# Optimization experiments

Measured on AMD Instinct MI355X. Metric: run time of the kernel, lower is better.

The kernel has to match this reference:

```python
import jax, jax.numpy as jnp
import numpy as np
import math

B, S, D, H, MLP, L = 4, 1024, 512, 8, 2048, 4
C = D // H  # head dim = 64
K_RATIO = 0.25
TOPK = max(1, min(S, int(math.ceil(K_RATIO * S))))  # 256
EPS = 1e-6


def layernorm(x, w, b):
    mu = jnp.mean(x, axis=-1, keepdims=True)
    var = jnp.mean(jnp.square(x - mu), axis=-1, keepdims=True)
    return (x - mu) * jax.lax.rsqrt(var + EPS) * w + b


def dwconv3(x, w):
    # x: (B, Ch, S), w: (Ch, 1, 3) depthwise conv, padding 1
    return jax.lax.conv_general_dilated(
        x, w, window_strides=(1,), padding=[(1, 1)],
        dimension_numbers=('NCH', 'OIH', 'NCH'),
        feature_group_count=x.shape[1])


def setup_inputs() -> dict:
    key = jax.random.key(0)
    ks = jax.random.split(key, 16)
    g = lambda k, shape, s=0.02: jax.random.normal(k, shape, jnp.float32) * s
    return {
        'x': jax.random.normal(ks[0], (B, S, D), jnp.float32),
        'pos_emb': g(ks[1], (1, S, D)),
        'ln1_w': jnp.ones((L, D), jnp.float32),
        'ln1_b': jnp.zeros((L, D), jnp.float32),
        'qkv_w': g(ks[2], (L, 3 * D, D)),
        'dw_w': g(ks[3], (L, 3 * D, 1, 3), 0.1),
        'temp': jnp.ones((L, H), jnp.float32),
        'proj_w': g(ks[4], (L, D, D)),
        'ln2_w': jnp.ones((L, D), jnp.float32),
        'ln2_b': jnp.zeros((L, D), jnp.float32),
        'mlp_w1': g(ks[5], (L, MLP, D)),
        'mlp_b1': g(ks[6], (L, MLP), 1e-6),
        'mlp_w2': g(ks[7], (L, D, MLP)),
        'mlp_b2': g(ks[8], (L, D), 1e-6),
        'lnf_w': jnp.ones((D,), jnp.float32),
        'lnf_b': jnp.zeros((D,), jnp.float32),
    }


def _block(x, ln1_w, ln1_b, qkv_w, dw_w, temp, proj_w, ln2_w, ln2_b,
           mlp_w1, mlp_b1, mlp_w2, mlp_b2):
    # x: (B, S, D)
    h = layernorm(x, ln1_w, ln1_b).swapaxes(1, 2)        # (B, D, S)
    qkv = jnp.einsum('od,bds->bos', qkv_w, h)            # (B, 3D, S) 1x1 conv
    qkv = dwconv3(qkv, dw_w)                             # depthwise k=3
    q, k, v = jnp.split(qkv, 3, axis=1)                  # each (B, D, S)
    # 'b (head c) s -> b head s c'
    to_heads = lambda t: t.reshape(B, H, C, S).transpose(0, 1, 3, 2)
    q, k, v = to_heads(q), to_heads(k), to_heads(v)      # (B, H, S, C)
    q = q / jnp.maximum(jnp.linalg.norm(q, axis=-1, keepdims=True), 1e-12)
    k = k / jnp.maximum(jnp.linalg.norm(k, axis=-1, keepdims=True), 1e-12)
    scores = jnp.einsum('bhsc,bhtc->bhst', q, k) * temp[None, :, None, None]
    # top-k per query row: keep entries >= k-th largest, mask rest to -inf
    kth = jax.lax.top_k(scores, TOPK)[0][..., -1:]       # (B, H, S, 1)
    sparse = jnp.where(scores >= kth, scores, -jnp.inf)
    sparse = jnp.clip(sparse, -10000.0, 10000.0)         # -inf -> -10000
    attn = jax.nn.softmax(sparse, axis=-1)
    out = jnp.einsum('bhst,bhtc->bhsc', attn, v)         # (B, H, S, C)
    out = out.transpose(0, 1, 3, 2).reshape(B, D, S)     # 'b head s c -> b (head c) s'
    out = jnp.einsum('od,bds->bos', proj_w, out)         # project_out 1x1 conv
    x = x + out.swapaxes(1, 2)                           # residual (dropout=0)
    y = layernorm(x, ln2_w, ln2_b)
    y = jax.nn.gelu(y @ mlp_w1.T + mlp_b1, approximate=False) @ mlp_w2.T + mlp_b2
    return x + y


def reference(x, pos_emb, ln1_w, ln1_b, qkv_w, dw_w, temp, proj_w,
              ln2_w, ln2_b, mlp_w1, mlp_b1, mlp_w2, mlp_b2, lnf_w, lnf_b):
    h = x + pos_emb
    for i in range(L):
        h = _block(h, ln1_w[i], ln1_b[i], qkv_w[i], dw_w[i], temp[i], proj_w[i],
                   ln2_w[i], ln2_b[i], mlp_w1[i], mlp_b1[i], mlp_w2[i], mlp_b2[i])
    return layernorm(h, lnf_w, lnf_b)
```

## Files before the change

### kernel.cpp

```cpp
#include <hip/hip_runtime.h>

#define NB   4
#define SEQ  1024
#define DIM  512
#define NH   8
#define HD   64
#define MLPD 2048
#define NL   4
#define TOPKK 256
#define QKVD 1536
#define QT   16

typedef short bh8 __attribute__((ext_vector_type(8)));
typedef float f32x4 __attribute__((ext_vector_type(4)));

__device__ __forceinline__ float b2f(unsigned short v) {
    return __uint_as_float(((unsigned)v) << 16);
}
__device__ __forceinline__ unsigned short f2b(float f) {
    unsigned u = __float_as_uint(f);
    u += 0x7FFFu + ((u >> 16) & 1u);
    return (unsigned short)(u >> 16);
}
__device__ __forceinline__ float ldin(const void* p, size_t i, int bf) {
    return bf ? b2f(((const unsigned short*)p)[i]) : ((const float*)p)[i];
}
__device__ __forceinline__ float wave_sum(float v) {
#pragma unroll
    for (int m = 32; m; m >>= 1) v += __shfl_xor(v, m);
    return v;
}
__device__ __forceinline__ unsigned f2key16(unsigned short u) {
    return (u & 0x8000u) ? (unsigned)((~u) & 0xFFFFu) : (unsigned)(u | 0x8000u);
}
__device__ __forceinline__ unsigned short key16b(unsigned k) {
    return (k & 0x8000u) ? (unsigned short)(k & 0x7FFFu)
                         : (unsigned short)((~k) & 0xFFFFu);
}
__device__ __forceinline__ unsigned cvtpk(float a, float b) {
    unsigned r;
    asm("v_cvt_pk_bf16_f32 %0, %1, %2" : "=v"(r) : "v"(a), "v"(b));
    return r;
}
__device__ __forceinline__ uint4 pack8(const float* __restrict__ p) {
    uint4 r;
    r.x = (unsigned)f2b(p[0]) | ((unsigned)f2b(p[1]) << 16);
    r.y = (unsigned)f2b(p[2]) | ((unsigned)f2b(p[3]) << 16);
    r.z = (unsigned)f2b(p[4]) | ((unsigned)f2b(p[5]) << 16);
    r.w = (unsigned)f2b(p[6]) | ((unsigned)f2b(p[7]) << 16);
    return r;
}
__device__ __forceinline__ void async16(unsigned short* lds, const unsigned short* g) {
    __builtin_amdgcn_global_load_lds(
        (const __attribute__((address_space(1))) unsigned int*)g,
        (__attribute__((address_space(3))) unsigned int*)lds, 16, 0, 0);
}


__global__ void detect_kernel(const unsigned short* __restrict__ ln1w,
                              int* __restrict__ flag) {
    if (threadIdx.x == 0 && blockIdx.x == 0)
        *flag = (ln1w[0] == 0x3F80u) ? 1 : 0;
}

__global__ __launch_bounds__(256) void wcvt_kernel(
    const void* __restrict__ W, unsigned short* __restrict__ out,
    int n, const int* __restrict__ dflag) {
    int bf = *dflag;
    int idx = blockIdx.x * 256 + threadIdx.x;
    if (idx < n) out[idx] = f2b(ldin(W, idx, bf));
}

__global__ __launch_bounds__(256) void addpos_kernel(
    const void* __restrict__ x, const void* __restrict__ pos,
    float* __restrict__ h, const int* __restrict__ dflag) {
    int bf = *dflag;
    int idx = blockIdx.x * 256 + threadIdx.x;
    int sd = idx & (SEQ * DIM - 1);
    h[idx] = ldin(x, idx, bf) + ldin(pos, sd, bf);
}

__global__ __launch_bounds__(256) void ln_kernel(
    const float* __restrict__ in, const void* __restrict__ w,
    const void* __restrict__ bb, size_t wo, unsigned short* __restrict__ out,
    const int* __restrict__ dflag) {
    int bf = *dflag;
    int tid = threadIdx.x;
    int lane = tid & 63, wid = tid >> 6;
    int row = blockIdx.x * 4 + wid;
    const float* p = in + (size_t)row * DIM + lane * 8;
    float4 x0 = *(const float4*)(p);
    float4 x1 = *(const float4*)(p + 4);
    float d[8] = {x0.x, x0.y, x0.z, x0.w, x1.x, x1.y, x1.z, x1.w};
    float s = (d[0] + d[1]) + (d[2] + d[3]) + (d[4] + d[5]) + (d[6] + d[7]);
    s = wave_sum(s);
    float mean = s * (1.0f / DIM);
    float q = 0.f;
#pragma unroll
    for (int j = 0; j < 8; ++j) {
        d[j] -= mean;
        q += d[j] * d[j];
    }
    q = wave_sum(q);
    float rs = rsqrtf(q * (1.0f / DIM) + 1e-6f);
    size_t eo = wo + lane * 8;
    unsigned short* o = out + (size_t)row * DIM + lane * 8;
    unsigned pw[4];
#pragma unroll
    for (int j = 0; j < 4; ++j) {
        float v0 = d[2 * j]     * rs * ldin(w, eo + 2 * j, bf)     + ldin(bb, eo + 2 * j, bf);
        float v1 = d[2 * j + 1] * rs * ldin(w, eo + 2 * j + 1, bf) + ldin(bb, eo + 2 * j + 1, bf);
        pw[j] = (unsigned)f2b(v0) | ((unsigned)f2b(v1) << 16);
    }
    *(uint4*)o = (uint4){pw[0], pw[1], pw[2], pw[3]};
}

__global__ __launch_bounds__(256) void lnf_kernel(
    const float* __restrict__ in, const void* __restrict__ w,
    const void* __restrict__ bb, void* __restrict__ out,
    const int* __restrict__ dflag) {
    int bf = *dflag;
    __shared__ float red[4];
    int row = blockIdx.x, tid = threadIdx.x;
    int lane = tid & 63, wid = tid >> 6;
    const float* p = in + (size_t)row * DIM;
    float x0 = p[tid], x1 = p[tid + 256];
    float s = wave_sum(x0 + x1);
    if (!lane) red[wid] = s;
    __syncthreads();
    float mean = (red[0] + red[1] + red[2] + red[3]) * (1.0f / DIM);
    float d0 = x0 - mean, d1 = x1 - mean;
    float q = wave_sum(d0 * d0 + d1 * d1);
    __syncthreads();
    if (!lane) red[wid] = q;
    __syncthreads();
    float var = (red[0] + red[1] + red[2] + red[3]) * (1.0f / DIM);
    float rs = rsqrtf(var + 1e-6f);
    float v0 = d0 * rs * ldin(w, tid, bf) + ldin(bb, tid, bf);
    float v1 = d1 * rs * ldin(w, tid + 256, bf) + ldin(bb, tid + 256, bf);
    size_t o = (size_t)row * DIM;
    if (bf) {
        ((unsigned short*)out)[o + tid]       = f2b(v0);
        ((unsigned short*)out)[o + tid + 256] = f2b(v1);
    } else {
        ((float*)out)[o + tid]       = v0;
        ((float*)out)[o + tid + 256] = v1;
    }
}

__global__ __launch_bounds__(256) void gemm_mfma_kernel(
    const unsigned short* __restrict__ A, const void* __restrict__ W, size_t wo,
    const void* __restrict__ bias, size_t bo, void* __restrict__ C,
    int M, int N, int K, int flags, const int* __restrict__ dflag) {
    int bf = *dflag;
    __shared__ unsigned short As[128 * 32];
    __shared__ unsigned short Bs[128 * 32];
    int tid = threadIdx.x;
    int w = tid >> 6, l = tid & 63;
    int n0 = blockIdx.x * 128, m0 = blockIdx.y * 128;
    int wm = (w >> 1) * 64, wn = (w & 1) * 64;
    int lq = l & 15, lk = l >> 4;

    int srow = w * 32 + (l >> 2);
    int cb = (l & 3) * 8;
    const unsigned short* aG = A + (size_t)(m0 + srow) * K + cb;
    size_t wb = wo + (size_t)(n0 + srow) * K + cb;
    unsigned short* sA0 = &As[w * 1024 + l * 8];
    unsigned short* sA1 = &As[w * 1024 + 512 + l * 8];
    unsigned short* sB0 = &Bs[w * 1024 + l * 8];
    unsigned short* sB1 = &Bs[w * 1024 + 512 + l * 8];

    f32x4 acc[4][4];
#pragma unroll
    for (int i = 0; i < 4; ++i)
#pragma unroll
        for (int j = 0; j < 4; ++j)
            acc[i][j] = (f32x4){0.f, 0.f, 0.f, 0.f};

    for (int k0 = 0; k0 < K; k0 += 32) {
        uint4 a0 = *(const uint4*)(aG + k0);
        uint4 a1 = *(const uint4*)(aG + 16 * K + k0);
        uint4 b0, b1;
        if (bf) {
            b0 = *(const uint4*)((const unsigned short*)W + wb + k0);
            b1 = *(const uint4*)((const unsigned short*)W + wb + 16 * K + k0);
        } else {
            b0 = pack8((const float*)W + wb + k0);
            b1 = pack8((const float*)W + wb + 16 * K + k0);
        }
        __syncthreads();
        *(uint4*)sA0 = a0;
        *(uint4*)sA1 = a1;
        *(uint4*)sB0 = b0;
        *(uint4*)sB1 = b1;
        __syncthreads();
        bh8 af[4], bw[4];
#pragma unroll
        for (int i = 0; i < 4; ++i) {
            af[i] = *(const bh8*)&As[(wm + i * 16 + lq) * 32 + lk * 8];
            bw[i] = *(const bh8*)&Bs[(wn + i * 16 + lq) * 32 + lk * 8];
        }
#pragma unroll
        for (int i = 0; i < 4; ++i)
#pragma unroll
            for (int j = 0; j < 4; ++j)
                acc[i][j] = __builtin_amdgcn_mfma_f32_16x16x32_bf16(
                    af[i], bw[j], acc[i][j], 0, 0, 0);
    }

    int lr4 = lk * 4;
#pragma unroll
    for (int i = 0; i < 4; ++i) {
#pragma unroll
        for (int j = 0; j < 4; ++j) {
            int n = n0 + wn + j * 16 + lq;
            float bv = (flags & 4) ? ldin(bias, bo + n, bf) : 0.0f;
#pragma unroll
            for (int r = 0; r < 4; ++r) {
                int m = m0 + wm + i * 16 + lr4 + r;
                float v = acc[i][j][r] + bv;
                if (flags & 2) v = 0.5f * v * (1.0f + erff(v * 0.70710678118654752f));
                size_t o = (size_t)m * N + n;
                if (flags & 1) ((float*)C)[o] += v;
                else           ((unsigned short*)C)[o] = f2b(v);
            }
        }
    }
}

__global__ __launch_bounds__(256) void gemm_mfma_n64_kernel(
    const unsigned short* __restrict__ A, const void* __restrict__ W, size_t wo,
    const void* __restrict__ bias, size_t bo, void* __restrict__ C,
    int M, int N, int K, int flags, const int* __restrict__ dflag) {
    int bf = *dflag;
    __shared__ unsigned short As[128 * 32];
    __shared__ unsigned short Bs[64 * 32];
    int tid = threadIdx.x;
    int w = tid >> 6, l = tid & 63;
    int n0 = blockIdx.x * 64, m0 = blockIdx.y * 128;
    int wm = (w >> 1) * 64, wn = (w & 1) * 32;
    int lq = l & 15, lk = l >> 4;

    int srowA = w * 32 + (l >> 2);
    int cb = (l & 3) * 8;
    const unsigned short* aG = A + (size_t)(m0 + srowA) * K + cb;
    int srowB = w * 16 + (l >> 2);
    size_t wb = wo + (size_t)(n0 + srowB) * K + cb;
    unsigned short* sA0 = &As[w * 1024 + l * 8];
    unsigned short* sA1 = &As[w * 1024 + 512 + l * 8];
    unsigned short* sB0 = &Bs[w * 512 + l * 8];

    f32x4 acc[4][2];
#pragma unroll
    for (int i = 0; i < 4; ++i) {
        acc[i][0] = (f32x4){0.f, 0.f, 0.f, 0.f};
        acc[i][1] = (f32x4){0.f, 0.f, 0.f, 0.f};
    }

    for (int k0 = 0; k0 < K; k0 += 32) {
        uint4 a0 = *(const uint4*)(aG + k0);
        uint4 a1 = *(const uint4*)(aG + 16 * K + k0);
        uint4 b0;
        if (bf) b0 = *(const uint4*)((const unsigned short*)W + wb + k0);
        else    b0 = pack8((const float*)W + wb + k0);
        __syncthreads();
        *(uint4*)sA0 = a0;
        *(uint4*)sA1 = a1;
        *(uint4*)sB0 = b0;
        __syncthreads();
        bh8 af[4], bw[2];
#pragma unroll
        for (int i = 0; i < 4; ++i)
            af[i] = *(const bh8*)&As[(wm + i * 16 + lq) * 32 + lk * 8];
        bw[0] = *(const bh8*)&Bs[(wn + lq) * 32 + lk * 8];
        bw[1] = *(const bh8*)&Bs[(wn + 16 + lq) * 32 + lk * 8];
#pragma unroll
        for (int i = 0; i < 4; ++i) {
            acc[i][0] = __builtin_amdgcn_mfma_f32_16x16x32_bf16(af[i], bw[0], acc[i][0], 0, 0, 0);
            acc[i][1] = __builtin_amdgcn_mfma_f32_16x16x32_bf16(af[i], bw[1], acc[i][1], 0, 0, 0);
        }
    }

    int lr4 = lk * 4;
#pragma unroll
    for (int i = 0; i < 4; ++i) {
#pragma unroll
        for (int j = 0; j < 2; ++j) {
            int n = n0 + wn + j * 16 + lq;
            float bv = (flags & 4) ? ldin(bias, bo + n, bf) : 0.0f;
#pragma unroll
            for (int r = 0; r < 4; ++r) {
                int m = m0 + wm + i * 16 + lr4 + r;
                float v = acc[i][j][r] + bv;
                if (flags & 2) v = 0.5f * v * (1.0f + erff(v * 0.70710678118654752f));
                size_t o = (size_t)m * N + n;
                if (flags & 1) ((float*)C)[o] += v;
                else           ((unsigned short*)C)[o] = f2b(v);
            }
        }
    }
}

__global__ __launch_bounds__(256) void gemm_n64_dlds_kernel(
    const unsigned short* __restrict__ A, const unsigned short* __restrict__ W, size_t wo,
    const void* __restrict__ bias, size_t bo, void* __restrict__ C,
    int M, int N, int K, int flags, const int* __restrict__ dflag) {
    __shared__ unsigned short As[128 * 32];
    __shared__ unsigned short Bs[64 * 32];
    int tid = threadIdx.x;
    int w = tid >> 6, l = tid & 63;
    int n0 = blockIdx.x * 64, m0 = blockIdx.y * 128;
    int kz = blockIdx.z;
    int Ks = K / (int)gridDim.z;
    int kbeg = kz * Ks, kend = kbeg + Ks;
    int wm = (w >> 1) * 64, wn = (w & 1) * 32;
    int lq = l & 15, lk = l >> 4;

    int srowA = w * 32 + (l >> 2);
    int srowB = w * 16 + (l >> 2);
    int cb = (l & 3) * 8;
    const unsigned short* aG = A + (size_t)(m0 + srowA) * K + cb;
    const unsigned short* wG = W + wo + (size_t)(n0 + srowB) * K + cb;
    unsigned short* lA0 = As + w * 1024;
    unsigned short* lA1 = As + w * 1024 + 512;
    unsigned short* lB0 = Bs + w * 512;

    f32x4 acc[4][2];
#pragma unroll
    for (int i = 0; i < 4; ++i) {
        acc[i][0] = (f32x4){0.f, 0.f, 0.f, 0.f};
        acc[i][1] = (f32x4){0.f, 0.f, 0.f, 0.f};
    }

    for (int k0 = kbeg; k0 < kend; k0 += 32) {
        __syncthreads();
        async16(lA0, aG + k0);
        async16(lA1, aG + 16 * K + k0);
        async16(lB0, wG + k0);
        __syncthreads();
        bh8 af[4], bw[2];
#pragma unroll
        for (int i = 0; i < 4; ++i)
            af[i] = *(const bh8*)&As[(wm + i * 16 + lq) * 32 + lk * 8];
        bw[0] = *(const bh8*)&Bs[(wn + lq) * 32 + lk * 8];
        bw[1] = *(const bh8*)&Bs[(wn + 16 + lq) * 32 + lk * 8];
#pragma unroll
        for (int i = 0; i < 4; ++i) {
            acc[i][0] = __builtin_amdgcn_mfma_f32_16x16x32_bf16(af[i], bw[0], acc[i][0], 0, 0, 0);
            acc[i][1] = __builtin_amdgcn_mfma_f32_16x16x32_bf16(af[i], bw[1], acc[i][1], 0, 0, 0);
        }
    }

    int bf = (flags & 4) ? *dflag : 0;
    int lr4 = lk * 4;
#pragma unroll
    for (int i = 0; i < 4; ++i) {
#pragma unroll
        for (int j = 0; j < 2; ++j) {
            int n = n0 + wn + j * 16 + lq;
            float bv = ((flags & 4) && kz == 0) ? ldin(bias, bo + n, bf) : 0.0f;
#pragma unroll
            for (int r = 0; r < 4; ++r) {
                int m = m0 + wm + i * 16 + lr4 + r;
                float v = acc[i][j][r] + bv;
                if (flags & 2) v = 0.5f * v * (1.0f + erff(v * 0.70710678118654752f));
                size_t o = (size_t)m * N + n;
                if (flags & 8)      atomicAdd(&((float*)C)[o], v);
                else if (flags & 1) ((float*)C)[o] += v;
                else                ((unsigned short*)C)[o] = f2b(v);
            }
        }
    }
}

__global__ __launch_bounds__(256) void dwqkv_kernel(
    const unsigned short* __restrict__ in, const void* __restrict__ w, size_t wo,
    const void* __restrict__ temp, size_t to,
    unsigned short* __restrict__ qn, unsigned short* __restrict__ Kc,
    unsigned short* __restrict__ Vt, const int* __restrict__ dflag) {
    int bf = *dflag;
    int tid = threadIdx.x;
    int g = tid >> 6, c = tid & 63;
    int gid = blockIdx.x * 4 + g;
    int h = gid & 7;
    int bs = gid >> 3;
    int s = bs & (SEQ - 1), b = bs >> 10;
    int bh = b * NH + h;
    const unsigned short* row = in + (size_t)bs * QKVD;
    float vals[3];
#pragma unroll
    for (int t = 0; t < 3; ++t) {
        int o = t * 512 + h * HD + c;
        float w0 = ldin(w, wo + o * 3 + 0, bf);
        float w1 = ldin(w, wo + o * 3 + 1, bf);
        float w2 = ldin(w, wo + o * 3 + 2, bf);
        float a = w1 * b2f(row[o]);
        if (s > 0)       a += w0 * b2f(row[o - QKVD]);
        if (s < SEQ - 1) a += w2 * b2f(row[o + QKVD]);
        vals[t] = a;
    }
    float qs = wave_sum(vals[0] * vals[0]);
    float ks = wave_sum(vals[1] * vals[1]);
    float t_ = ldin(temp, to + h, bf);
    qn[(size_t)bs * DIM + h * HD + c] = f2b(vals[0] / fmaxf(sqrtf(qs), 1e-12f) * t_);
    Kc[((size_t)bh * SEQ + s) * HD + c] = f2b(vals[1] / fmaxf(sqrtf(ks), 1e-12f));
    Vt[(((size_t)bh * 32 + (s >> 5)) * HD + c) * 32 + (s & 31)] = f2b(vals[2]);
}

__global__ __launch_bounds__(256) void attn_kernel(
    const unsigned short* __restrict__ q, const unsigned short* __restrict__ Kc,
    const unsigned short* __restrict__ Vt, unsigned short* __restrict__ outp) {
    __shared__ __align__(16) unsigned short sc16[QT * 1024];

    int tid = threadIdx.x;
    int w = tid >> 6, l = tid & 63;
    int lq = l & 15, lk = l >> 4;
    int bid = blockIdx.x;
    int qt = (bid >> 3) & 63;
    int bh = ((bid >> 9) << 3) | (bid & 7);
    int h = bh & 7;
    int b = bh >> 3;

    const unsigned short* qp = q + (size_t)(b * SEQ + qt * QT + lq) * DIM + h * HD + lk * 8;
    bh8 aq0 = *(const bh8*)(qp);
    bh8 aq1 = *(const bh8*)(qp + 32);

    int swz = ((lq ^ (lq >> 2)) & 7) << 1;

    const unsigned short* Kbh = Kc + (size_t)bh * SEQ * HD;
    unsigned short* srowq = sc16 + lq * 1024;
    for (int kb = 0; kb < 16; kb += 2) {
        int key0 = (w * 16 + kb) * 16;
        const unsigned short* kp0 = Kbh + (size_t)(key0 + lq) * HD + lk * 8;
        const unsigned short* kp1 = kp0 + 16 * HD;
        bh8 b0 = *(const bh8*)(kp0);
        bh8 b1 = *(const bh8*)(kp0 + 32);
        bh8 b2 = *(const bh8*)(kp1);
        bh8 b3 = *(const bh8*)(kp1 + 32);
        f32x4 a0 = {0.f, 0.f, 0.f, 0.f};
        f32x4 a1 = {0.f, 0.f, 0.f, 0.f};
        a0 = __builtin_amdgcn_mfma_f32_16x16x32_bf16(b0, aq0, a0, 0, 0, 0);
        a0 = __builtin_amdgcn_mfma_f32_16x16x32_bf16(b1, aq1, a0, 0, 0, 0);
        a1 = __builtin_amdgcn_mfma_f32_16x16x32_bf16(b2, aq0, a1, 0, 0, 0);
        a1 = __builtin_amdgcn_mfma_f32_16x16x32_bf16(b3, aq1, a1, 0, 0, 0);
        int c0 = (key0 >> 2) + lk;
        uint2 w0 = {cvtpk(a0[0], a0[1]), cvtpk(a0[2], a0[3])};
        uint2 w1 = {cvtpk(a1[0], a1[1]), cvtpk(a1[2], a1[3])};
        *(uint2*)&srowq[(c0 ^ swz) << 2]       = w0;
        *(uint2*)&srowq[((c0 + 4) ^ swz) << 2] = w1;
    }
    __syncthreads();

    for (int rr = 0; rr < 4; rr += 2) {
        int rowA = w * 4 + rr;
        unsigned short* sAr = sc16 + rowA * 1024;
        unsigned short* sBr = sc16 + (rowA + 1) * 1024;
        uint4 ra0 = *(const uint4*)&sAr[l * 8];
        uint4 ra1 = *(const uint4*)&sAr[512 + l * 8];
        uint4 rb0 = *(const uint4*)&sBr[l * 8];
        uint4 rb1 = *(const uint4*)&sBr[512 + l * 8];
        unsigned wa[8] = {ra0.x, ra0.y, ra0.z, ra0.w, ra1.x, ra1.y, ra1.z, ra1.w};
        unsigned wb[8] = {rb0.x, rb0.y, rb0.z, rb0.w, rb1.x, rb1.y, rb1.z, rb1.w};
        float va[16], vb[16];
#pragma unroll
        for (int j = 0; j < 8; ++j) {
            va[2 * j]     = __uint_as_float(wa[j] << 16);
            va[2 * j + 1] = __uint_as_float(wa[j] & 0xFFFF0000u);
            vb[2 * j]     = __uint_as_float(wb[j] << 16);
            vb[2 * j + 1] = __uint_as_float(wb[j] & 0xFFFF0000u);
        }
        float ma = va[0], mb = vb[0];
#pragma unroll
        for (int j = 1; j < 16; ++j) {
            ma = fmaxf(ma, va[j]);
            mb = fmaxf(mb, vb[j]);
        }
#pragma unroll
        for (int off = 1; off < 64; off <<= 1) {
            ma = fmaxf(ma, __shfl_xor(ma, off));
            mb = fmaxf(mb, __shfl_xor(mb, off));
        }
        ma = fminf(fmaxf(ma, -10000.f), 10000.f);
        mb = fminf(fmaxf(mb, -10000.f), 10000.f);
        unsigned Ta = 0, Tb = 0;
        for (int bit = 15; bit >= 0; --bit) {
            unsigned ca = Ta | (1u << bit), cb = Tb | (1u << bit);
            float tfa = b2f(key16b(ca)), tfb = b2f(key16b(cb));
            unsigned cna = 0, cnb = 0;
#pragma unroll
            for (int j = 0; j < 16; ++j) {
                cna += (unsigned)__popcll(__ballot(va[j] >= tfa));
                cnb += (unsigned)__popcll(__ballot(vb[j] >= tfb));
            }
            if (cna >= TOPKK) Ta = ca;
            if (cnb >= TOPKK) Tb = cb;
        }
        float ka = b2f(key16b(Ta)), kb = b2f(key16b(Tb));
        float sa = 0.f, sb = 0.f;
#pragma unroll
        for (int j = 0; j < 16; ++j) {
            float aa = fminf(fmaxf(va[j], -10000.f), 10000.f);
            float ab = fminf(fmaxf(vb[j], -10000.f), 10000.f);
            float ea = (va[j] >= ka) ? __expf(aa - ma) : 0.0f;
            float eb = (vb[j] >= kb) ? __expf(ab - mb) : 0.0f;
            sa += ea; sb += eb;
            va[j] = ea; vb[j] = eb;
        }
#pragma unroll
        for (int off = 1; off < 64; off <<= 1) {
            sa += __shfl_xor(sa, off);
            sb += __shfl_xor(sb, off);
        }
        float ia = 1.0f / sa, ib = 1.0f / sb;
        unsigned pa[8], pb[8];
#pragma unroll
        for (int j = 0; j < 8; ++j) {
            pa[j] = cvtpk(va[2 * j] * ia, va[2 * j + 1] * ia);
            pb[j] = cvtpk(vb[2 * j] * ib, vb[2 * j + 1] * ib);
        }
        *(uint4*)&sAr[l * 8]       = (uint4){pa[0], pa[1], pa[2], pa[3]};
        *(uint4*)&sAr[512 + l * 8] = (uint4){pa[4], pa[5], pa[6], pa[7]};
        *(uint4*)&sBr[l * 8]       = (uint4){pb[0], pb[1], pb[2], pb[3]};
        *(uint4*)&sBr[512 + l * 8] = (uint4){pb[4], pb[5], pb[6], pb[7]};
    }
    __syncthreads();

    {
        const unsigned short* Vbh = Vt + (size_t)bh * SEQ * HD;
        const unsigned short* prow = sc16 + lq * 1024;
        f32x4 oacc = {0.f, 0.f, 0.f, 0.f};
        for (int tc = 0; tc < 32; tc += 2) {
            const unsigned short* vp0 = Vbh + (size_t)tc * 2048 + (w * 16 + lq) * 32 + lk * 8;
            bh8 bv0 = *(const bh8*)(vp0);
            bh8 bv1 = *(const bh8*)(vp0 + 2048);
            bh8 ap0 = *(const bh8*)&prow[((tc * 8 + lk * 2) ^ swz) << 2];
            bh8 ap1 = *(const bh8*)&prow[(((tc + 1) * 8 + lk * 2) ^ swz) << 2];
            oacc = __builtin_amdgcn_mfma_f32_16x16x32_bf16(ap0, bv0, oacc, 0, 0, 0);
            oacc = __builtin_amdgcn_mfma_f32_16x16x32_bf16(ap1, bv1, oacc, 0, 0, 0);
        }
#pragma unroll
        for (int r = 0; r < 4; ++r) {
            int qrow = lk * 4 + r;
            outp[((size_t)(b * SEQ + qt * QT + qrow)) * DIM + h * HD + w * 16 + lq] = f2b(oacc[r]);
        }
    }
}

extern "C" void kernel_launch(void* const* d_in, const int* in_sizes, int n_in,
                              void* d_out, int out_size, void* d_ws, size_t ws_size,
                              hipStream_t stream) {
    (void)in_sizes; (void)n_in; (void)out_size;
    const void* x     = d_in[0];
    const void* pos   = d_in[1];
    const void* ln1w  = d_in[2];
    const void* ln1b  = d_in[3];
    const void* qkvw  = d_in[4];
    const void* dww   = d_in[5];
    const void* temp  = d_in[6];
    const void* projw = d_in[7];
    const void* ln2w  = d_in[8];
    const void* ln2b  = d_in[9];
    const void* w1    = d_in[10];
    const void* b1    = d_in[11];
    const void* w2    = d_in[12];
    const void* b2    = d_in[13];
    const void* lnfw  = d_in[14];
    const void* lnfb  = d_in[15];

    float* wsf = (float*)d_ws;
    const size_t M1 = (size_t)1024 * 1024;
    float*          h    = wsf;
    unsigned short* bn   = (unsigned short*)(wsf + 2 * M1);
    unsigned short* C2   = (unsigned short*)(wsf + 3 * M1);
    unsigned short* Vt   = (unsigned short*)(wsf + 6 * M1);
    unsigned short* Kc   = (unsigned short*)(wsf + 7 * M1);
    unsigned short* Mb   = C2;
    int*            flag = (int*)(wsf + 9 * M1);
    unsigned short* Wc   = (unsigned short*)(wsf + 9 * M1 + 16);

    const int MTOK  = NB * SEQ;
    const int nQKVW = NL * QKVD * DIM;
    const int nPROJ = NL * DIM * DIM;
    const int nW1   = NL * MLPD * DIM;
    const int nW2   = NL * DIM * MLPD;
    const size_t wcElems = (size_t)nQKVW + nPROJ + nW1 + nW2;
    const int big = ws_size >= ((9 * M1 + 16) * 4 + wcElems * 2);

    unsigned short* WcQ  = Wc;
    unsigned short* WcP  = Wc + nQKVW;
    unsigned short* WcW1 = Wc + nQKVW + nPROJ;
    unsigned short* WcW2 = Wc + nQKVW + nPROJ + (size_t)nW1;

    detect_kernel<<<1, 64, 0, stream>>>((const unsigned short*)ln1w, flag);
    addpos_kernel<<<(NB * SEQ * DIM) / 256, 256, 0, stream>>>(x, pos, h, flag);

    if (big) {
        wcvt_kernel<<<nQKVW / 256, 256, 0, stream>>>(qkvw, WcQ, nQKVW, flag);
        wcvt_kernel<<<nPROJ / 256, 256, 0, stream>>>(projw, WcP, nPROJ, flag);
        wcvt_kernel<<<nW1 / 256, 256, 0, stream>>>(w1, WcW1, nW1, flag);
        wcvt_kernel<<<nW2 / 256, 256, 0, stream>>>(w2, WcW2, nW2, flag);
    }

    for (int l = 0; l < NL; ++l) {
        ln_kernel<<<MTOK / 4, 256, 0, stream>>>(h, ln1w, ln1b, (size_t)l * DIM, bn, flag);
        if (big) {
            gemm_n64_dlds_kernel<<<dim3(QKVD / 64, MTOK / 128, 1), 256, 0, stream>>>(
                bn, WcQ, (size_t)l * QKVD * DIM, nullptr, 0, C2,
                MTOK, QKVD, DIM, 0, flag);
        } else {
            gemm_mfma_kernel<<<dim3(QKVD / 128, MTOK / 128), 256, 0, stream>>>(
                bn, qkvw, (size_t)l * QKVD * DIM, nullptr, 0, C2,
                MTOK, QKVD, DIM, 0, flag);
        }
        dwqkv_kernel<<<(NB * SEQ * NH) / 4, 256, 0, stream>>>(
            C2, dww, (size_t)l * QKVD * 3, temp, (size_t)l * NH, bn, Kc, Vt, flag);
        attn_kernel<<<NB * NH * (SEQ / QT), 256, 0, stream>>>(bn, Kc, Vt, bn);
        if (big) {
            gemm_n64_dlds_kernel<<<dim3(DIM / 64, MTOK / 128, 2), 256, 0, stream>>>(
                bn, WcP, (size_t)l * DIM * DIM, nullptr, 0, h,
                MTOK, DIM, DIM, 8, flag);
        } else {
            gemm_mfma_n64_kernel<<<dim3(DIM / 64, MTOK / 128), 256, 0, stream>>>(
                bn, projw, (size_t)l * DIM * DIM, nullptr, 0, h,
                MTOK, DIM, DIM, 1, flag);
        }
        ln_kernel<<<MTOK / 4, 256, 0, stream>>>(h, ln2w, ln2b, (size_t)l * DIM, bn, flag);
        if (big) {
            gemm_n64_dlds_kernel<<<dim3(MLPD / 64, MTOK / 128, 1), 256, 0, stream>>>(
                bn, WcW1, (size_t)l * MLPD * DIM, b1, (size_t)l * MLPD, Mb,
                MTOK, MLPD, DIM, 2 | 4, flag);
            gemm_n64_dlds_kernel<<<dim3(DIM / 64, MTOK / 128, 2), 256, 0, stream>>>(
                Mb, WcW2, (size_t)l * DIM * MLPD, b2, (size_t)l * DIM, h,
                MTOK, DIM, MLPD, 8 | 4, flag);
        } else {
            gemm_mfma_kernel<<<dim3(MLPD / 128, MTOK / 128), 256, 0, stream>>>(
                bn, w1, (size_t)l * MLPD * DIM, b1, (size_t)l * MLPD, Mb,
                MTOK, MLPD, DIM, 2 | 4, flag);
            gemm_mfma_n64_kernel<<<dim3(DIM / 64, MTOK / 128), 256, 0, stream>>>(
                Mb, w2, (size_t)l * DIM * MLPD, b2, (size_t)l * DIM, h,
                MTOK, DIM, MLPD, 1 | 4, flag);
        }
    }

    lnf_kernel<<<MTOK, 256, 0, stream>>>(h, lnfw, lnfb, d_out, flag);
}
```

Before: 1.015 ms.

## Double-buffer LDS tiles in split-K n64 GEMM to overlap loads with MFMA

Doubles the shared-memory A/B tile buffers in the n64 direct-to-LDS GEMM kernel. The next K-tile is issued asynchronously into the alternate buffer while MFMAs run on the current one. This removes one of the two barriers per iteration. The aim is to hide global-to-LDS latency behind compute, at the cost of twice the LDS footprint, which may reduce occupancy.

Result: no change. 1.010 ms (median of 2 runs) (-0.5%).

```diff
diff --git a/kernel.cpp b/kernel.cpp
--- a/kernel.cpp
+++ b/kernel.cpp
@@ -305,25 +305,23 @@
     const unsigned short* __restrict__ A, const unsigned short* __restrict__ W, size_t wo,
     const void* __restrict__ bias, size_t bo, void* __restrict__ C,
     int M, int N, int K, int flags, const int* __restrict__ dflag) {
-    __shared__ unsigned short As[128 * 32];
-    __shared__ unsigned short Bs[64 * 32];
+    __shared__ unsigned short As[2][128 * 32];
+    __shared__ unsigned short Bs[2][64 * 32];
     int tid = threadIdx.x;
     int w = tid >> 6, l = tid & 63;
     int n0 = blockIdx.x * 64, m0 = blockIdx.y * 128;
     int kz = blockIdx.z;
     int Ks = K / (int)gridDim.z;
-    int kbeg = kz * Ks, kend = kbeg + Ks;
+    int kbeg = kz * Ks;
+    int nt = Ks / 32;
     int wm = (w >> 1) * 64, wn = (w & 1) * 32;
     int lq = l & 15, lk = l >> 4;
 
     int srowA = w * 32 + (l >> 2);
     int srowB = w * 16 + (l >> 2);
     int cb = (l & 3) * 8;
-    const unsigned short* aG = A + (size_t)(m0 + srowA) * K + cb;
-    const unsigned short* wG = W + wo + (size_t)(n0 + srowB) * K + cb;
-    unsigned short* lA0 = As + w * 1024;
-    unsigned short* lA1 = As + w * 1024 + 512;
-    unsigned short* lB0 = Bs + w * 512;
+    const unsigned short* aG = A + (size_t)(m0 + srowA) * K + cb + kbeg;
+    const unsigned short* wG = W + wo + (size_t)(n0 + srowB) * K + cb + kbeg;
 
     f32x4 acc[4][2];
 #pragma unroll
@@ -332,23 +330,32 @@
         acc[i][1] = (f32x4){0.f, 0.f, 0.f, 0.f};
     }
 
-    for (int k0 = kbeg; k0 < kend; k0 += 32) {
-        __syncthreads();
-        async16(lA0, aG + k0);
-        async16(lA1, aG + 16 * K + k0);
-        async16(lB0, wG + k0);
-        __syncthreads();
+    async16(&As[0][w * 1024], aG);
+    async16(&As[0][w * 1024 + 512], aG + 16 * K);
+    async16(&Bs[0][w * 512], wG);
+
+    int cur = 0;
+    for (int t = 0; t < nt; ++t) {
+        asm volatile("s_waitcnt vmcnt(0)" ::: "memory");
+        __builtin_amdgcn_s_barrier();
+        if (t + 1 < nt) {
+            int k1 = (t + 1) * 32;
+            async16(&As[cur ^ 1][w * 1024], aG + k1);
+            async16(&As[cur ^ 1][w * 1024 + 512], aG + 16 * K + k1);
+            async16(&Bs[cur ^ 1][w * 512], wG + k1);
+        }
         bh8 af[4], bw[2];
 #pragma unroll
         for (int i = 0; i < 4; ++i)
-            af[i] = *(const bh8*)&As[(wm + i * 16 + lq) * 32 + lk * 8];
-        bw[0] = *(const bh8*)&Bs[(wn + lq) * 32 + lk * 8];
-        bw[1] = *(const bh8*)&Bs[(wn + 16 + lq) * 32 + lk * 8];
+            af[i] = *(const bh8*)&As[cur][(wm + i * 16 + lq) * 32 + lk * 8];
+        bw[0] = *(const bh8*)&Bs[cur][(wn + lq) * 32 + lk * 8];
+        bw[1] = *(const bh8*)&Bs[cur][(wn + 16 + lq) * 32 + lk * 8];
 #pragma unroll
         for (int i = 0; i < 4; ++i) {
             acc[i][0] = __builtin_amdgcn_mfma_f32_16x16x32_bf16(af[i], bw[0], acc[i][0], 0, 0, 0);
             acc[i][1] = __builtin_amdgcn_mfma_f32_16x16x32_bf16(af[i], bw[1], acc[i][1], 0, 0, 0);
         }
+        cur ^= 1;
     }
 
     int bf = (flags & 4) ? *dflag : 0;
```
